# Performance work log

Measured on AMD Instinct MI355X. Metric: run time of the kernel, lower is better.

Reference implementation:

```python
import jax, jax.numpy as jnp
import numpy as np
from math import sqrt

B, IN_C, OUT_C, H, W, WDIM, K = 16, 512, 512, 64, 64, 512, 3
EPS = 1e-8
LRELU_SLOPE = 0.2


def setup_inputs() -> dict:
    key = jax.random.key(0)
    ks = jax.random.split(key, 5)
    return {
        "x": jax.random.normal(ks[0], (B, IN_C, H, W), dtype=jnp.float32),
        "w": jax.random.normal(ks[1], (B, WDIM), dtype=jnp.float32),
        "noise": jax.random.normal(ks[2], (B, 1, H, W), dtype=jnp.float32),
        "linear_w": jax.random.normal(ks[3], (IN_C, WDIM), dtype=jnp.float32),
        "linear_b": jnp.ones((IN_C,), dtype=jnp.float32),
        "conv_w": jax.random.normal(ks[4], (OUT_C, IN_C, K, K), dtype=jnp.float32),
        "scale_noise": jnp.zeros((OUT_C,), dtype=jnp.float32),
        "bias": jnp.zeros((OUT_C,), dtype=jnp.float32),
    }


def reference(x, w, noise, linear_w, linear_b, conv_w, scale_noise, bias):
    # EqualizerStraights: equalized-lr linear, scale = 1/sqrt(w_dim)
    s = w @ (linear_w * (1.0 / sqrt(WDIM))).T + linear_b  # [b, in_c]
    # Weight_Demod: equalized conv weight, scale = 1/sqrt(in_c*k*k)
    base_w = conv_w * (1.0 / sqrt(IN_C * K * K))  # [out, in, k, k]
    weights = base_w[None] * s[:, None, :, None, None]  # [b, out, in, k, k]
    sigma_inv = jax.lax.rsqrt(
        jnp.sum(weights * weights, axis=(2, 3, 4), keepdims=True) + EPS)
    weights = weights * sigma_inv

    def conv1(xi, wi):  # xi [in,h,w], wi [out,in,k,k]
        return jax.lax.conv_general_dilated(
            xi[None], wi, window_strides=(1, 1), padding="SAME",
            dimension_numbers=("NCHW", "OIHW", "NCHW"))[0]

    y = jax.vmap(conv1)(x, weights)  # [b, out, h, w]
    y = y + scale_noise[None, :, None, None] * noise
    return jax.nn.leaky_relu(y + bias[None, :, None, None], negative_slope=LRELU_SLOPE)
```

## Files before the change

### kernel.cpp

```cpp
#include <hip/hip_runtime.h>
#include <hip/hip_bf16.h>
#include <stdint.h>

typedef __bf16 bf16_t;
typedef __bf16 bf16x8 __attribute__((ext_vector_type(8)));
typedef short short8 __attribute__((ext_vector_type(8)));
typedef float f32x4 __attribute__((ext_vector_type(4)));

#define RS512  0.044194173824159216f
#define RS4608 0.014731391274719739f

__global__ void k_style(const float* __restrict__ w, const float* __restrict__ lw,
                        const float* __restrict__ lb, float* __restrict__ s) {
  int b = blockIdx.y;
  int c = blockIdx.x * 256 + threadIdx.x;
  const float4* wr = (const float4*)(w + b * 512);
  const float4* lr = (const float4*)(lw + (size_t)c * 512);
  float acc = 0.f;
#pragma unroll 4
  for (int d = 0; d < 128; ++d) {
    float4 a = wr[d], q = lr[d];
    acc += a.x * q.x + a.y * q.y + a.z * q.z + a.w * q.w;
  }
  s[b * 512 + c] = acc * RS512 + lb[c];
}

__global__ void k_wprep(const float* __restrict__ cw, float* __restrict__ wsq,
                        bf16_t* __restrict__ bw) {
  int idx = blockIdx.x * 256 + threadIdx.x;
  float v[9];
  float ss = 0.f;
#pragma unroll
  for (int t = 0; t < 9; ++t) {
    float x = cw[(size_t)idx * 9 + t] * RS4608;
    v[t] = x;
    ss += x * x;
  }
  wsq[idx] = ss;
#pragma unroll
  for (int t = 0; t < 9; ++t) bw[((size_t)t << 18) + idx] = (bf16_t)v[t];
}

__global__ void k_sigma(const float* __restrict__ s, const float* __restrict__ wsq,
                        float* __restrict__ sinv) {
  __shared__ float s2[512];
  int b = blockIdx.y;
  int o = blockIdx.x * 256 + threadIdx.x;
  for (int i = threadIdx.x; i < 512; i += 256) {
    float v = s[b * 512 + i];
    s2[i] = v * v;
  }
  __syncthreads();
  const float4* qr = (const float4*)(wsq + (size_t)o * 512);
  float acc = 0.f;
#pragma unroll 4
  for (int d = 0; d < 128; ++d) {
    float4 q = qr[d];
    acc += q.x * s2[4 * d] + q.y * s2[4 * d + 1] + q.z * s2[4 * d + 2] + q.w * s2[4 * d + 3];
  }
  sinv[b * 512 + o] = rsqrtf(acc + 1e-8f);
}

__global__ void k_xt(const float* __restrict__ x, const float* __restrict__ s,
                     bf16_t* __restrict__ xt) {
  int ic = blockIdx.x, h = blockIdx.y, b = blockIdx.z;
  __shared__ __align__(16) bf16_t tile[8192];
  int t = threadIdx.x;
  int wcol = t & 63;
  int g = t >> 6;
#pragma unroll
  for (int blk = 0; blk < 4; ++blk) {
    int grp = blk * 4 + g;
    bf16x8 vec;
#pragma unroll
    for (int k = 0; k < 8; ++k) {
      int i = ic * 128 + grp * 8 + k;
      float v = x[(((size_t)b * 512 + i) * 64 + h) * 64 + wcol] * s[b * 512 + i];
      vec[k] = (bf16_t)v;
    }
    int chunk = grp ^ (wcol & 15);
    *(bf16x8*)((char*)tile + wcol * 256 + chunk * 16) = vec;
  }
  __syncthreads();
#pragma unroll
  for (int j = 0; j < 4; ++j) {
    int flat = j * 256 + t;
    int wo = flat >> 4, ig8 = flat & 15;
    int chunk = ig8 ^ (wo & 15);
    bf16x8 v = *(bf16x8*)((char*)tile + wo * 256 + chunk * 16);
    *(bf16x8*)(xt + (((size_t)b * 64 + h) * 64 + wo) * 512 + ic * 128 + ig8 * 8) = v;
  }
}

#define AS1 __attribute__((address_space(1)))
#define AS3 __attribute__((address_space(3)))

__device__ __forceinline__ void gl16(const void* g, void* l) {
  __builtin_amdgcn_global_load_lds((const AS1 void*)g, (AS3 void*)l, 16, 0, 0);
}

__global__ __launch_bounds__(256) void k_conv(
    const bf16_t* __restrict__ xt, const bf16_t* __restrict__ bw,
    const float* __restrict__ sinv, const float* __restrict__ noise,
    const float* __restrict__ snz, const float* __restrict__ bias,
    float* __restrict__ out) {
  __shared__ __align__(16) char lds[49152];

  const int t = threadIdx.x;
  const int rp = blockIdx.x;
  const int o0 = blockIdx.y * 128;
  const int b = blockIdx.z;
  const int h0 = rp * 2;
  const int lane = t & 63;
  const int wv = t >> 6;
  const int wm = wv >> 1, wn = wv & 1;

  const bf16_t* xb_base = xt + (size_t)b * 2097152;

  f32x4 acc[4][4] = {};

  auto stageX = [&](int c, int buf) {
    char* ldst = lds + buf * 16384 + (wv << 10);
    const bf16_t* g0 = xb_base + (size_t)(t >> 2) * 512 + c * 32 + (t & 3) * 8;
#pragma unroll
    for (int r = 0; r < 4; ++r) {
      int gr = h0 - 1 + r;
      if ((unsigned)gr < 64u) {
        gl16(g0 + (size_t)gr * 32768, ldst + r * 4096);
      } else {
        *(f32x4*)(lds + buf * 16384 + r * 4096 + t * 16) = (f32x4)0.f;
      }
    }
  };

  auto stageW = [&](int c, int tap, int buf) {
    char* ldst = lds + 32768 + buf * 8192 + (wv << 10);
    const bf16_t* g0 = bw + ((size_t)tap << 18) + (size_t)o0 * 512 + c * 32;
#pragma unroll
    for (int j = 0; j < 2; ++j) {
      int f = j * 256 + t;
      gl16(g0 + (size_t)(f >> 2) * 512 + (f & 3) * 8, ldst + j * 4096);
    }
  };

  stageX(0, 0);
  stageW(0, 0, 0);
  __syncthreads();

  for (int c = 0; c < 16; ++c) {
    const int xbuf = c & 1;
#pragma unroll
    for (int tap = 0; tap < 9; ++tap) {
      const int wb = (c + tap) & 1;
      if (tap < 8) {
        stageW(c, tap + 1, wb ^ 1);
      } else if (c < 15) {
        stageW(c + 1, 0, wb ^ 1);
        stageX(c + 1, xbuf ^ 1);
      }
      const int ky = tap / 3, kx = tap % 3;

      const char* wbase = lds + 32768 + wb * 8192 +
                          (wm * 64 + (lane & 15)) * 64 + (lane >> 4) * 16;
      bf16x8 af[4];
#pragma unroll
      for (int mi = 0; mi < 4; ++mi) af[mi] = *(const bf16x8*)(wbase + mi * 16 * 64);

      const char* xbase = lds + xbuf * 16384 + (wn + ky) * 4096 + (lane >> 4) * 16;
      bf16x8 bfr[4];
#pragma unroll
      for (int ni = 0; ni < 4; ++ni) {
        int icol = ni * 16 + (lane & 15) + kx - 1;
        bool valid = (unsigned)icol < 64u;
        int ic2 = valid ? icol : 0;
        short8 xv = *(const short8*)(xbase + ic2 * 64);
        if (!valid) xv = (short8)0;
        bfr[ni] = __builtin_bit_cast(bf16x8, xv);
      }
#pragma unroll
      for (int mi = 0; mi < 4; ++mi)
#pragma unroll
        for (int ni = 0; ni < 4; ++ni)
          acc[mi][ni] =
              __builtin_amdgcn_mfma_f32_16x16x32_bf16(af[mi], bfr[ni], acc[mi][ni], 0, 0, 0);
      __syncthreads();
    }
  }

  const float* sb = sinv + b * 512;
  const int orow_base = o0 + wm * 64 + ((lane >> 4) << 2);
  const int prow = h0 + wn;
  float nz[4];
#pragma unroll
  for (int ni = 0; ni < 4; ++ni)
    nz[ni] = noise[(size_t)b * 4096 + prow * 64 + ni * 16 + (lane & 15)];
#pragma unroll
  for (int mi = 0; mi < 4; ++mi) {
#pragma unroll
    for (int r = 0; r < 4; ++r) {
      int o = orow_base + mi * 16 + r;
      float sv = sb[o];
      float nw = snz[o];
      float bv = bias[o];
      float* orow = out + (((size_t)b * 512 + o) * 64 + prow) * 64;
#pragma unroll
      for (int ni = 0; ni < 4; ++ni) {
        int col = ni * 16 + (lane & 15);
        float v = acc[mi][ni][r] * sv + nw * nz[ni] + bv;
        orow[col] = v > 0.f ? v : 0.2f * v;
      }
    }
  }
}

extern "C" void kernel_launch(void* const* d_in, const int* in_sizes, int n_in,
                              void* d_out, int out_size, void* d_ws, size_t ws_size,
                              hipStream_t stream) {
  const float* x     = (const float*)d_in[0];
  const float* w     = (const float*)d_in[1];
  const float* noise = (const float*)d_in[2];
  const float* lw    = (const float*)d_in[3];
  const float* lb    = (const float*)d_in[4];
  const float* cw    = (const float*)d_in[5];
  const float* snz   = (const float*)d_in[6];
  const float* bias  = (const float*)d_in[7];
  float* out = (float*)d_out;

  char* ws = (char*)d_ws;
  bf16_t* xt   = (bf16_t*)ws;
  bf16_t* bw   = (bf16_t*)(ws + 67108864);
  float*  s    = (float*)(ws + 71827456);
  float*  sinv = (float*)(ws + 71860224);
  float*  wsq  = (float*)(ws + 71892992);

  k_style<<<dim3(2, 16), 256, 0, stream>>>(w, lw, lb, s);
  k_wprep<<<dim3(1024), 256, 0, stream>>>(cw, wsq, bw);
  k_sigma<<<dim3(2, 16), 256, 0, stream>>>(s, wsq, sinv);
  k_xt<<<dim3(4, 64, 16), 256, 0, stream>>>(x, s, xt);
  k_conv<<<dim3(32, 4, 16), 256, 0, stream>>>(xt, bw, sinv, noise, snz, bias, out);
}
```

Baseline: 358.0 us.

## Prepack weights into MFMA fragment layout, load directly to registers, enlarge spatial tile

Weights are pre-laid out in MFMA A-fragment order so each wave loads them straight from global memory into registers, double-buffered across taps, instead of staging them through LDS. Each block now covers four output rows instead of two, so the per-wave accumulator grows to 4x8 tiles and every weight fragment is reused twice as often. The input tile is XOR-swizzled to cut LDS bank conflicts, and the barrier runs once per channel chunk instead of once per tap. The cost is much higher register pressure: there are 128 accumulator VGPRs plus weight buffers under launch_bounds(256,2), and the grid is halved, which may lower occupancy.

```diff
diff --git a/kernel.cpp b/kernel.cpp
--- a/kernel.cpp
+++ b/kernel.cpp
@@ -26,8 +26,9 @@
 }
 
 __global__ void k_wprep(const float* __restrict__ cw, float* __restrict__ wsq,
-                        bf16_t* __restrict__ bw) {
+                        bf16_t* __restrict__ bwf) {
   int idx = blockIdx.x * 256 + threadIdx.x;
+  int o = idx >> 9, i = idx & 511;
   float v[9];
   float ss = 0.f;
 #pragma unroll
@@ -37,8 +38,13 @@
     ss += x * x;
   }
   wsq[idx] = ss;
-#pragma unroll
-  for (int t = 0; t < 9; ++t) bw[((size_t)t << 18) + idx] = (bf16_t)v[t];
+  int lane = (o & 15) | (((i >> 3) & 3) << 4);
+  int base_blk = (i >> 5) * 32 + (o >> 4);
+#pragma unroll
+  for (int t = 0; t < 9; ++t) {
+    size_t e = ((size_t)(t * 512 + base_blk) << 9) + lane * 8 + (i & 7);
+    bwf[e] = (bf16_t)v[t];
+  }
 }
 
 __global__ void k_sigma(const float* __restrict__ s, const float* __restrict__ wsq,
@@ -88,7 +94,9 @@
     int wo = flat >> 4, ig8 = flat & 15;
     int chunk = ig8 ^ (wo & 15);
     bf16x8 v = *(bf16x8*)((char*)tile + wo * 256 + chunk * 16);
-    *(bf16x8*)(xt + (((size_t)b * 64 + h) * 64 + wo) * 512 + ic * 128 + ig8 * 8) = v;
+    int c32 = (ig8 >> 2);
+    int slot = (ig8 & 3) ^ ((wo >> 1) & 3);
+    *(bf16x8*)(xt + (((size_t)b * 64 + h) * 64 + wo) * 512 + ic * 128 + c32 * 32 + slot * 8) = v;
   }
 }
 
@@ -99,115 +107,117 @@
   __builtin_amdgcn_global_load_lds((const AS1 void*)g, (AS3 void*)l, 16, 0, 0);
 }
 
-__global__ __launch_bounds__(256) void k_conv(
-    const bf16_t* __restrict__ xt, const bf16_t* __restrict__ bw,
+__global__ __launch_bounds__(256, 2) void k_conv(
+    const bf16_t* __restrict__ xt, const bf16_t* __restrict__ bwf,
     const float* __restrict__ sinv, const float* __restrict__ noise,
     const float* __restrict__ snz, const float* __restrict__ bias,
     float* __restrict__ out) {
   __shared__ __align__(16) char lds[49152];
 
   const int t = threadIdx.x;
-  const int rp = blockIdx.x;
-  const int o0 = blockIdx.y * 128;
+  const int rq = blockIdx.x;
+  const int oy = blockIdx.y;
   const int b = blockIdx.z;
-  const int h0 = rp * 2;
+  const int h0 = rq * 4;
   const int lane = t & 63;
   const int wv = t >> 6;
-  const int wm = wv >> 1, wn = wv & 1;
-
-  const bf16_t* xb_base = xt + (size_t)b * 2097152;
-
-  f32x4 acc[4][4] = {};
+  const int wm = wv >> 1;
+  const int wn = wv & 1;
+
+  const bf16_t* xb = xt + (size_t)b * 2097152;
+
+  f32x4 acc[4][8] = {};
+
+  const bf16_t* wfb = bwf + (((size_t)(oy * 8 + wm * 4)) << 9) + lane * 8;
 
   auto stageX = [&](int c, int buf) {
-    char* ldst = lds + buf * 16384 + (wv << 10);
-    const bf16_t* g0 = xb_base + (size_t)(t >> 2) * 512 + c * 32 + (t & 3) * 8;
-#pragma unroll
-    for (int r = 0; r < 4; ++r) {
+    char* ldst = lds + buf * 24576 + (wv << 10);
+    const bf16_t* g0 = xb + (size_t)(t >> 2) * 512 + c * 32 + (t & 3) * 8;
+#pragma unroll
+    for (int r = 0; r < 6; ++r) {
       int gr = h0 - 1 + r;
-      if ((unsigned)gr < 64u) {
-        gl16(g0 + (size_t)gr * 32768, ldst + r * 4096);
-      } else {
-        *(f32x4*)(lds + buf * 16384 + r * 4096 + t * 16) = (f32x4)0.f;
-      }
+      if ((unsigned)gr < 64u) gl16(g0 + (size_t)gr * 32768, ldst + r * 4096);
     }
   };
 
-  auto stageW = [&](int c, int tap, int buf) {
-    char* ldst = lds + 32768 + buf * 8192 + (wv << 10);
-    const bf16_t* g0 = bw + ((size_t)tap << 18) + (size_t)o0 * 512 + c * 32;
-#pragma unroll
-    for (int j = 0; j < 2; ++j) {
-      int f = j * 256 + t;
-      gl16(g0 + (size_t)(f >> 2) * 512 + (f & 3) * 8, ldst + j * 4096);
-    }
+  if (h0 == 0) {
+    *(f32x4*)(lds + t * 16) = (f32x4)0.f;
+    *(f32x4*)(lds + 24576 + t * 16) = (f32x4)0.f;
+  }
+  if (h0 == 60) {
+    *(f32x4*)(lds + 5 * 4096 + t * 16) = (f32x4)0.f;
+    *(f32x4*)(lds + 24576 + 5 * 4096 + t * 16) = (f32x4)0.f;
+  }
+
+  bf16x8 wcur[4], wnxt[4];
+  auto loadW = [&](int tap, int c, bf16x8* d) {
+#pragma unroll
+    for (int mi = 0; mi < 4; ++mi)
+      d[mi] = *(const bf16x8*)(wfb + (((size_t)((tap * 16 + c) * 32 + mi)) << 9));
   };
 
   stageX(0, 0);
-  stageW(0, 0, 0);
+  loadW(0, 0, wcur);
   __syncthreads();
 
   for (int c = 0; c < 16; ++c) {
     const int xbuf = c & 1;
+    if (c < 15) stageX(c + 1, xbuf ^ 1);
+    const char* xb0 = lds + xbuf * 24576;
 #pragma unroll
     for (int tap = 0; tap < 9; ++tap) {
-      const int wb = (c + tap) & 1;
-      if (tap < 8) {
-        stageW(c, tap + 1, wb ^ 1);
-      } else if (c < 15) {
-        stageW(c + 1, 0, wb ^ 1);
-        stageX(c + 1, xbuf ^ 1);
-      }
+      if (tap < 8) loadW(tap + 1, c, wnxt);
+      else if (c < 15) loadW(0, c + 1, wnxt);
       const int ky = tap / 3, kx = tap % 3;
-
-      const char* wbase = lds + 32768 + wb * 8192 +
-                          (wm * 64 + (lane & 15)) * 64 + (lane >> 4) * 16;
-      bf16x8 af[4];
-#pragma unroll
-      for (int mi = 0; mi < 4; ++mi) af[mi] = *(const bf16x8*)(wbase + mi * 16 * 64);
-
-      const char* xbase = lds + xbuf * 16384 + (wn + ky) * 4096 + (lane >> 4) * 16;
-      bf16x8 bfr[4];
-#pragma unroll
-      for (int ni = 0; ni < 4; ++ni) {
-        int icol = ni * 16 + (lane & 15) + kx - 1;
+      bf16x8 bfr[8];
+#pragma unroll
+      for (int ni = 0; ni < 8; ++ni) {
+        const int rslot = wn * 2 + (ni >> 2) + ky;
+        int icol = (ni & 3) * 16 + (lane & 15) + kx - 1;
         bool valid = (unsigned)icol < 64u;
         int ic2 = valid ? icol : 0;
-        short8 xv = *(const short8*)(xbase + ic2 * 64);
+        int slot = (lane >> 4) ^ ((ic2 >> 1) & 3);
+        short8 xv = *(const short8*)(xb0 + rslot * 4096 + ic2 * 64 + slot * 16);
         if (!valid) xv = (short8)0;
         bfr[ni] = __builtin_bit_cast(bf16x8, xv);
       }
 #pragma unroll
       for (int mi = 0; mi < 4; ++mi)
 #pragma unroll
-        for (int ni = 0; ni < 4; ++ni)
+        for (int ni = 0; ni < 8; ++ni)
           acc[mi][ni] =
-              __builtin_amdgcn_mfma_f32_16x16x32_bf16(af[mi], bfr[ni], acc[mi][ni], 0, 0, 0);
-      __syncthreads();
-    }
+              __builtin_amdgcn_mfma_f32_16x16x32_bf16(wcur[mi], bfr[ni], acc[mi][ni], 0, 0, 0);
+#pragma unroll
+      for (int mi = 0; mi < 4; ++mi) wcur[mi] = wnxt[mi];
+    }
+    __syncthreads();
   }
 
   const float* sb = sinv + b * 512;
-  const int orow_base = o0 + wm * 64 + ((lane >> 4) << 2);
-  const int prow = h0 + wn;
-  float nz[4];
-#pragma unroll
-  for (int ni = 0; ni < 4; ++ni)
-    nz[ni] = noise[(size_t)b * 4096 + prow * 64 + ni * 16 + (lane & 15)];
+  const int og = oy * 128 + wm * 64 + ((lane >> 4) << 2);
+  const int colb = lane & 15;
+  float nzv[8];
+#pragma unroll
+  for (int ni = 0; ni < 8; ++ni) {
+    int prow = h0 + wn * 2 + (ni >> 2);
+    int col = (ni & 3) * 16 + colb;
+    nzv[ni] = noise[(size_t)b * 4096 + prow * 64 + col];
+  }
 #pragma unroll
   for (int mi = 0; mi < 4; ++mi) {
 #pragma unroll
     for (int r = 0; r < 4; ++r) {
-      int o = orow_base + mi * 16 + r;
+      int o = og + mi * 16 + r;
       float sv = sb[o];
       float nw = snz[o];
       float bv = bias[o];
-      float* orow = out + (((size_t)b * 512 + o) * 64 + prow) * 64;
-#pragma unroll
-      for (int ni = 0; ni < 4; ++ni) {
-        int col = ni * 16 + (lane & 15);
-        float v = acc[mi][ni][r] * sv + nw * nz[ni] + bv;
-        orow[col] = v > 0.f ? v : 0.2f * v;
+      float* obase = out + ((size_t)b * 512 + o) * 4096;
+#pragma unroll
+      for (int ni = 0; ni < 8; ++ni) {
+        int prow = h0 + wn * 2 + (ni >> 2);
+        int col = (ni & 3) * 16 + colb;
+        float v = acc[mi][ni][r] * sv + nw * nzv[ni] + bv;
+        obase[prow * 64 + col] = v > 0.f ? v : 0.2f * v;
       }
     }
   }
@@ -228,14 +238,14 @@
 
   char* ws = (char*)d_ws;
   bf16_t* xt   = (bf16_t*)ws;
-  bf16_t* bw   = (bf16_t*)(ws + 67108864);
+  bf16_t* bwf  = (bf16_t*)(ws + 67108864);
   float*  s    = (float*)(ws + 71827456);
   float*  sinv = (float*)(ws + 71860224);
   float*  wsq  = (float*)(ws + 71892992);
 
   k_style<<<dim3(2, 16), 256, 0, stream>>>(w, lw, lb, s);
-  k_wprep<<<dim3(1024), 256, 0, stream>>>(cw, wsq, bw);
+  k_wprep<<<dim3(1024), 256, 0, stream>>>(cw, wsq, bwf);
   k_sigma<<<dim3(2, 16), 256, 0, stream>>>(s, wsq, sinv);
   k_xt<<<dim3(4, 64, 16), 256, 0, stream>>>(x, s, xt);
-  k_conv<<<dim3(32, 4, 16), 256, 0, stream>>>(xt, bw, sinv, noise, snz, bias, out);
-}
+  k_conv<<<dim3(16, 4, 16), 256, 0, stream>>>(xt, bwf, sinv, noise, snz, bias, out);
+}
```

New measurement: 411.3 us. +14.9%, slower.
